# Optimization experiments

Hardware: AMD Instinct MI355X
Metric: run time of the kernel (lower is better)

Reference implementation:

```python
import jax, jax.numpy as jnp
import numpy as np

B, C, N, K, G = 4, 128, 4096, 9, 4


def setup_inputs() -> dict:
    key = jax.random.key(0)
    ks = jax.random.split(key, 4)
    s = 0.05
    return {
        "features": jax.random.normal(ks[0], (B, C, N, 1), jnp.float32),
        # Attn.linear: Conv2d(2C -> C, 1x1)
        "w_lin": jax.random.normal(ks[1], (C, 2 * C), jnp.float32) * s,
        "b_lin": jnp.zeros((C,), jnp.float32),
        # atten_weight_conv: Linear(C -> K*G)
        "w_aw": jax.random.normal(ks[2], (K * G, C), jnp.float32) * s,
        "b_aw": jnp.zeros((K * G,), jnp.float32),
        # GroupNorm(4, C)
        "gn_g": jnp.ones((C,), jnp.float32),
        "gn_b": jnp.zeros((C,), jnp.float32),
        # conv: Conv2d(C -> C, 1x1) + BatchNorm2d(C)
        "conv_w": jax.random.normal(ks[3], (C, C), jnp.float32) * s,
        "conv_b": jnp.zeros((C,), jnp.float32),
        "bn_g": jnp.ones((C,), jnp.float32),
        "bn_b": jnp.zeros((C,), jnp.float32),
    }


def reference(features, w_lin, b_lin, w_aw, b_aw, gn_g, gn_b, conv_w, conv_b, bn_g, bn_b):
    B, C, N, _ = features.shape
    K, G = 9, 4
    Cg = C // G  # 32 channels per group
    EPS = 1e-5

    x = features[..., 0]                       # [B,C,N]
    # ---- KNN graph (negative squared distance, top-k) ----
    xx = jnp.sum(x * x, axis=1)                # [B,N]
    inner = jnp.einsum('bcn,bcm->bnm', x, x)   # [B,N,N]
    pd = 2.0 * inner - xx[:, :, None] - xx[:, None, :]
    idx = jax.lax.top_k(pd, K)[1]              # [B,N,K]

    # ---- edge feature gather: cat(x, x - x_neighbor) ----
    xt = x.transpose(0, 2, 1)                  # [B,N,C]
    b_ix = jnp.arange(B)[:, None, None]
    nbr = xt[b_ix, idx]                        # [B,N,K,C]
    ctr = jnp.broadcast_to(xt[:, :, None, :], (B, N, K, C))
    edge = jnp.concatenate([ctr, ctr - nbr], axis=-1)   # [B,N,K,2C]

    # ---- Attn.linear (1x1 conv == per-position linear) ----
    feat = jnp.einsum('bnke,ce->bnkc', edge, w_lin) + b_lin  # [B,N,K,C]

    # ---- grouped channel attention (4 groups of 32) ----
    fg = feat.reshape(B, N, K, G, Cg)
    scores = jnp.einsum('bnkgc,bnjgc->bngkj', fg, fg) / np.sqrt(32.0)
    s = jax.nn.softmax(scores, axis=-1)        # [B,N,G,K,K]
    attn = jnp.einsum('bngkj,bnjgc->bngkc', s, jax.nn.elu(fg))  # [B,N,G,K,Cg]

    # ---- attention weights over neighbors ----
    aw = jnp.einsum('bnc,dc->bnd', xt, w_aw) + b_aw          # [B,N,K*G]
    aw = jax.nn.softmax(aw.reshape(B, N, G, K), axis=-1)     # [B,N,G,K]

    # ---- weighted neighbor combine ----
    lf = jnp.einsum('bngk,bngkc->bngc', aw, attn)            # [B,N,G,Cg]
    lf = lf.transpose(0, 2, 3, 1).reshape(B, C, N, 1)        # [B,C,N,1]

    # ---- GroupNorm(4, C) over residual ----
    y = lf + features
    yg = y.reshape(B, G, Cg * N)
    mu = yg.mean(-1, keepdims=True)
    var = yg.var(-1, keepdims=True)
    yn = ((yg - mu) / jnp.sqrt(var + EPS)).reshape(B, C, N, 1)
    yn = yn * gn_g[None, :, None, None] + gn_b[None, :, None, None]

    # ---- 1x1 conv + BatchNorm (training-mode batch stats) + ReLU ----
    z = jnp.einsum('oc,bcnk->bonk', conv_w, yn) + conv_b[None, :, None, None]
    m = z.mean(axis=(0, 2, 3), keepdims=True)
    v = z.var(axis=(0, 2, 3), keepdims=True)
    z = (z - m) / jnp.sqrt(v + EPS) * bn_g[None, :, None, None] + bn_b[None, :, None, None]
    return jax.nn.relu(z)
```

## Files before the change

### kernel.cpp

```cpp
#include <hip/hip_runtime.h>
#include <hip/hip_bf16.h>
#include <cstddef>

#define NPTS 4096
#define CCH  128
#define KNN  9
#define GRP  4
#define BB   4
#define OFF_XT    0u
#define OFF_XX    2097152u
#define OFF_XHI   2113536u
#define OFF_IDX   3162112u
#define OFF_O     3309568u
#define OFF_Y     8159232u
#define OFF_GNP   10256384u
#define OFF_GNA   10387456u
#define OFF_GND   10387968u
#define OFF_WP    10388480u
#define OFF_BIASP 10454016u
#define OFF_BNSUM 10454528u
#define OFF_BNSQ  10454656u
#define OFF_BNSC  10454784u
#define OFF_BNSH  10454912u

using bf16x8 = __attribute__((ext_vector_type(8))) short;
using f32x4  = __attribute__((ext_vector_type(4))) float;

#define CE(a, b) { float _h = fmaxf(a, b); b = fminf(a, b); a = _h; }

#define SENT_BITS 0xFF7FF000u

__global__ void k_transpose(const float* __restrict__ x, float* __restrict__ xt,
                            __hip_bfloat16* __restrict__ xhi, float* __restrict__ xx) {
  __shared__ float t[32][33];
  int tx = threadIdx.x, ty = threadIdx.y;
  int n0 = blockIdx.x * 32, c0 = blockIdx.y * 32, b = blockIdx.z;
  float v = x[((size_t)b * CCH + c0 + ty) * NPTS + n0 + tx];
  t[ty][tx] = v;
  __syncthreads();
  float tv = t[tx][ty];
  size_t R = (size_t)b * NPTS + n0 + ty;
  int c = c0 + tx;
  xt[R * CCH + c] = tv;
  int g = c >> 3, w = c & 7;
  int sc = (((g ^ ((n0 + ty) & 15)) << 3) | w);
  xhi[R * CCH + sc] = __float2bfloat16(tv);
  if (ty == 0) {
    float s = 0.f;
    #pragma unroll
    for (int k = 0; k < 32; k++) { float u = t[k][tx]; s += u * u; }
    atomicAdd(&xx[b * NPTS + n0 + tx], s);
  }
}

__device__ __forceinline__ void select_chunk(int c, int wave, int quad,
                                             const f32x4 (&acc)[2][2],
                                             float (&top8)[2][8]) {
  const unsigned cbase = (unsigned)(c * 128 + wave * 32 + quad * 4);
  #pragma unroll
  for (int qt = 0; qt < 2; qt++) {
    float k[8];
    #pragma unroll
    for (int ct = 0; ct < 2; ct++)
      #pragma unroll
      for (int r = 0; r < 4; r++) {
        unsigned u = __float_as_uint(acc[ct][qt][r]);
        k[ct * 4 + r] = __uint_as_float((u & 0xFFFFF000u) |
                                        (cbase + (unsigned)(ct * 16 + r)));
      }
    CE(k[0],k[1]) CE(k[2],k[3]) CE(k[4],k[5]) CE(k[6],k[7])
    CE(k[0],k[2]) CE(k[1],k[3]) CE(k[4],k[6]) CE(k[5],k[7])
    CE(k[1],k[2]) CE(k[5],k[6])
    CE(k[0],k[4]) CE(k[1],k[5]) CE(k[2],k[6]) CE(k[3],k[7])
    CE(k[2],k[4]) CE(k[3],k[5])
    CE(k[1],k[2]) CE(k[3],k[4]) CE(k[5],k[6])
    float t[8];
    #pragma unroll
    for (int i = 0; i < 8; i++) t[i] = fmaxf(top8[qt][i], k[7 - i]);
    CE(t[0],t[4]) CE(t[1],t[5]) CE(t[2],t[6]) CE(t[3],t[7])
    CE(t[0],t[2]) CE(t[1],t[3]) CE(t[4],t[6]) CE(t[5],t[7])
    CE(t[0],t[1]) CE(t[2],t[3]) CE(t[4],t[5]) CE(t[6],t[7])
    #pragma unroll
    for (int i = 0; i < 8; i++) top8[qt][i] = t[i];
  }
}

__device__ __forceinline__ void load_chunk(const short* __restrict__ xb,
                                           const int (&aoff)[2][4], int c,
                                           bf16x8 (&af)[2][4]) {
  const short* cb = xb + c * (128 * CCH);
  #pragma unroll
  for (int ct = 0; ct < 2; ct++)
    #pragma unroll
    for (int ks = 0; ks < 4; ks++)
      af[ct][ks] = *(const bf16x8*)(cb + aoff[ct][ks]);
}

__launch_bounds__(256, 3)
__global__ void k_knn(const short* __restrict__ xhi, const float* __restrict__ xx,
                      float* __restrict__ cand) {
  __shared__ short Qs[32 * 136];
  __shared__ float XXs[1408];
  const int tid = threadIdx.x;
  const int wave = tid >> 6, lane = tid & 63;
  const int quad = lane >> 4, m = lane & 15;
  const int b = blockIdx.y;
  const int q0 = blockIdx.x * 32;
  const int z = blockIdx.z;
  const int ch0 = z * 11;
  const int cnt = (z == 2) ? 10 : 11;
  const short* xb = xhi + (size_t)b * NPTS * CCH;
  const float* xxb = xx + (b << 12);

  {
    int f = tid;
    #pragma unroll
    for (int it = 0; it < 2; it++, f += 256) {
      int row = f >> 4, s = f & 15;
      bf16x8 v = *(const bf16x8*)(xb + (size_t)(q0 + row) * CCH + s * 8);
      int g = s ^ (row & 15);
      *(bf16x8*)&Qs[row * 136 + g * 8] = v;
    }
    const float4* src4 = (const float4*)(xxb + ch0 * 128);
    float4* dst4 = (float4*)XXs;
    int nf4 = cnt * 32;
    for (int i = tid; i < nf4; i += 256) {
      float4 v = src4[i];
      dst4[i] = make_float4(-0.5f * v.x, -0.5f * v.y, -0.5f * v.z, -0.5f * v.w);
    }
  }

  int aoff[2][4];
  #pragma unroll
  for (int ct = 0; ct < 2; ct++)
    #pragma unroll
    for (int ks = 0; ks < 4; ks++)
      aoff[ct][ks] = (wave * 32 + ct * 16 + m) * CCH + (((ks * 4 + quad) ^ m) * 8);

  float top8[2][8];
  #pragma unroll
  for (int qt = 0; qt < 2; qt++)
    #pragma unroll
    for (int p = 0; p < 8; p++) top8[qt][p] = __uint_as_float(SENT_BITS);

  f32x4 acc[2][2];
  bf16x8 bufA[2][4], bufB[2][4];

  unsigned qoff = (unsigned)(m * 272 + quad * 16);
  const unsigned xbase = (unsigned)(wave * 128 + quad * 16);

  load_chunk(xb, aoff, ch0, bufA);
  __syncthreads();

  auto mfma_lds = [&](const bf16x8 (&af)[2][4], int crel) {
    unsigned xo = xbase + (unsigned)crel * 512u;
    f32x4 ci0 = *(const f32x4*)((const char*)XXs + xo);
    f32x4 ci1 = *(const f32x4*)((const char*)XXs + xo + 64);
    acc[0][0] = ci0; acc[0][1] = ci0; acc[1][0] = ci1; acc[1][1] = ci1;
    #pragma unroll
    for (int ks = 0; ks < 4; ks++) {
      bf16x8 qv0 = *(const bf16x8*)((const char*)Qs + qoff + ks * 64);
      bf16x8 qv1 = *(const bf16x8*)((const char*)Qs + qoff + 4352 + ks * 64);
      acc[0][0] = __builtin_amdgcn_mfma_f32_16x16x32_bf16(af[0][ks], qv0, acc[0][0], 0, 0, 0);
      acc[0][1] = __builtin_amdgcn_mfma_f32_16x16x32_bf16(af[0][ks], qv1, acc[0][1], 0, 0, 0);
      acc[1][0] = __builtin_amdgcn_mfma_f32_16x16x32_bf16(af[1][ks], qv0, acc[1][0], 0, 0, 0);
      acc[1][1] = __builtin_amdgcn_mfma_f32_16x16x32_bf16(af[1][ks], qv1, acc[1][1], 0, 0, 0);
    }
  };

  int c = ch0;
  for (; c + 1 < ch0 + cnt; c += 2) {
    load_chunk(xb, aoff, c + 1, bufB);
    if (c > ch0) select_chunk(c - 1, wave, quad, acc, top8);
    asm volatile("" : "+v"(qoff));
    mfma_lds(bufA, c - ch0);
    if (c + 2 < ch0 + cnt) load_chunk(xb, aoff, c + 2, bufA);
    select_chunk(c, wave, quad, acc, top8);
    asm volatile("" : "+v"(qoff));
    mfma_lds(bufB, c + 1 - ch0);
  }
  if (cnt & 1) {
    select_chunk(ch0 + cnt - 2, wave, quad, acc, top8);
    asm volatile("" : "+v"(qoff));
    mfma_lds(bufA, cnt - 1);
  }
  select_chunk(ch0 + cnt - 1, wave, quad, acc, top8);

  int slot = wave * 4 + quad;
  #pragma unroll
  for (int qt = 0; qt < 2; qt++) {
    int q = q0 + qt * 16 + m;
    float* dst = cand + ((size_t)((b << 12) + q) * 48 + z * 16 + slot) * 8;
    #pragma unroll
    for (int p = 0; p < 8; p++) dst[p] = top8[qt][p];
  }
}

__launch_bounds__(256)
__global__ void k_rerank(const float* __restrict__ cand, const float* __restrict__ xt,
                         const float* __restrict__ xx, int* __restrict__ idxOut) {
  __shared__ __align__(16) float arr[4][128];
  __shared__ int selS[4][16];
  __shared__ float keyS[4][16];
  int tid = threadIdx.x, wave = tid >> 6, lane = tid & 63;
  int qg = blockIdx.x * 4 + wave;
  int b = qg >> 12;
  const float* src = cand + (size_t)qg * 384;
  if (lane < 16) {
    const float* pa = src + lane * 8;
    float4 a0 = *(const float4*)pa,         a1 = *(const float4*)(pa + 4);
    float4 b0 = *(const float4*)(pa + 128), b1 = *(const float4*)(pa + 132);
    float4 c0 = *(const float4*)(pa + 256), c1 = *(const float4*)(pa + 260);
    float t[8];
    t[0] = fmaxf(a0.x, b1.w); t[1] = fmaxf(a0.y, b1.z);
    t[2] = fmaxf(a0.z, b1.y); t[3] = fmaxf(a0.w, b1.x);
    t[4] = fmaxf(a1.x, b0.w); t[5] = fmaxf(a1.y, b0.z);
    t[6] = fmaxf(a1.z, b0.y); t[7] = fmaxf(a1.w, b0.x);
    CE(t[0],t[4]) CE(t[1],t[5]) CE(t[2],t[6]) CE(t[3],t[7])
    CE(t[0],t[2]) CE(t[1],t[3]) CE(t[4],t[6]) CE(t[5],t[7])
    CE(t[0],t[1]) CE(t[2],t[3]) CE(t[4],t[5]) CE(t[6],t[7])
    arr[wave][lane * 8 + 0] = fmaxf(t[0], c1.w);
    arr[wave][lane * 8 + 1] = fmaxf(t[1], c1.z);
    arr[wave][lane * 8 + 2] = fmaxf(t[2], c1.y);
    arr[wave][lane * 8 + 3] = fmaxf(t[3], c1.x);
    arr[wave][lane * 8 + 4] = fmaxf(t[4], c0.w);
    arr[wave][lane * 8 + 5] = fmaxf(t[5], c0.z);
    arr[wave][lane * 8 + 6] = fmaxf(t[6], c0.y);
    arr[wave][lane * 8 + 7] = fmaxf(t[7], c0.x);
  }
  __syncthreads();
  float e1 = arr[wave][lane], e2 = arr[wave][lane + 64];
  int r1 = 0, r2 = 0;
  #pragma unroll 8
  for (int f = 0; f < 128; f += 4) {
    float4 fv = *(const float4*)&arr[wave][f];
    r1 += (fv.x > e1) + (fv.y > e1) + (fv.z > e1) + (fv.w > e1);
    r2 += (fv.x > e2) + (fv.y > e2) + (fv.z > e2) + (fv.w > e2);
  }
  if (r1 < 16) selS[wave][r1] = (int)(__float_as_uint(e1) & 0xFFFu);
  if (r2 < 16) selS[wave][r2] = (int)(__float_as_uint(e2) & 0xFFFu);
  __syncthreads();
  int cnum = lane >> 2, part = lane & 3;
  int cidx = selS[wave][cnum];
  const float* rq = xt + (size_t)qg * CCH;
  const float* rc = xt + ((size_t)(b << 12) + cidx) * CCH;
  float dot = 0.f;
  #pragma unroll
  for (int j = 0; j < 8; j++) {
    float4 a4 = *(const float4*)&rq[part * 32 + j * 4];
    float4 c4 = *(const float4*)&rc[part * 32 + j * 4];
    dot += a4.x * c4.x + a4.y * c4.y + a4.z * c4.z + a4.w * c4.w;
  }
  dot += __shfl_xor(dot, 1);
  dot += __shfl_xor(dot, 2);
  if (part == 0)
    keyS[wave][cnum] = fmaf(2.f, dot, -xx[(b << 12) + cidx]);
  __syncthreads();
  if (lane < 16) {
    float k = keyS[wave][lane]; int i = selS[wave][lane];
    int r = 0;
    #pragma unroll
    for (int f = 0; f < 16; f++) {
      float fk = keyS[wave][f]; int fi = selS[wave][f];
      r += (fk > k) || (fk == k && fi < i);
    }
    if (r < 9) idxOut[(size_t)qg * 9 + r] = i;
  }
}

__launch_bounds__(256)
__global__ void k_linear(const float* __restrict__ xt, const float* __restrict__ w_lin,
                         const float* __restrict__ b_lin, const float* __restrict__ w_aw,
                         const float* __restrict__ b_aw, float* __restrict__ O) {
  __shared__ __align__(16) float Xs[64 * 132];
  __shared__ __align__(16) float Ws[64 * 132];
  int tid = threadIdx.x;
  int tx = tid & 15, ty = tid >> 4;
  int p0 = blockIdx.x * 64, o0 = blockIdx.y * 64;
  #pragma unroll
  for (int i = 0; i < 8; i++) {
    int flat = tid + i * 256; int r = flat >> 5, c4 = flat & 31;
    *(float4*)&Xs[r * 132 + c4 * 4] = *(const float4*)&xt[(size_t)(p0 + r) * CCH + c4 * 4];
  }
  #pragma unroll
  for (int i = 0; i < 8; i++) {
    int flat = tid + i * 256; int r = flat >> 5, c4 = flat & 31;
    int o = o0 + r; float4 v;
    if (o < 128) {
      float4 a = *(const float4*)&w_lin[(size_t)o * 256 + c4 * 4];
      float4 c = *(const float4*)&w_lin[(size_t)o * 256 + 128 + c4 * 4];
      v = make_float4(a.x + c.x, a.y + c.y, a.z + c.z, a.w + c.w);
    } else if (o < 256) {
      v = *(const float4*)&w_lin[(size_t)(o - 128) * 256 + 128 + c4 * 4];
    } else if (o < 292) {
      v = *(const float4*)&w_aw[(size_t)(o - 256) * 128 + c4 * 4];
    } else v = make_float4(0.f, 0.f, 0.f, 0.f);
    *(float4*)&Ws[r * 132 + c4 * 4] = v;
  }
  __syncthreads();
  float acc[4][4] = {};
  #pragma unroll 2
  for (int kq = 0; kq < 32; kq++) {
    float4 xa[4], wb[4];
    #pragma unroll
    for (int i = 0; i < 4; i++) xa[i] = *(const float4*)&Xs[(ty * 4 + i) * 132 + kq * 4];
    #pragma unroll
    for (int j = 0; j < 4; j++) wb[j] = *(const float4*)&Ws[(tx + 16 * j) * 132 + kq * 4];
    #pragma unroll
    for (int i = 0; i < 4; i++)
      #pragma unroll
      for (int j = 0; j < 4; j++)
        acc[i][j] += xa[i].x * wb[j].x + xa[i].y * wb[j].y + xa[i].z * wb[j].z + xa[i].w * wb[j].w;
  }
  #pragma unroll
  for (int j = 0; j < 4; j++) {
    int o = o0 + tx + 16 * j;
    if (o < 292) {
      float bias = (o < 128) ? b_lin[o] : ((o < 256) ? 0.f : b_aw[o - 256]);
      #pragma unroll
      for (int i = 0; i < 4; i++)
        O[(size_t)(p0 + ty * 4 + i) * 296 + o] = acc[i][j] + bias;
    }
  }
}

__launch_bounds__(256)
__global__ void k_attn(const float* __restrict__ O, const int* __restrict__ idxArr,
                       const float* __restrict__ xt, float* __restrict__ Y,
                       float* __restrict__ gnPart) {
  __shared__ __align__(16) float fF[4][1188];
  __shared__ __align__(16) float scS[4][432];
  __shared__ float awS[4][48];
  __shared__ float w9S[4][48];
  __shared__ int tI[45], tJ[45];
  int tid = threadIdx.x;
  int wave = tid >> 6, l = tid & 63;
  int pos = blockIdx.x * 4 + wave;
  int b = pos >> 12;
  if (tid == 0) {
    int p = 0;
    for (int i = 0; i < 9; i++) for (int j = i; j < 9; j++) { tI[p] = i; tJ[p] = j; p++; }
  }
  int nbr[9];
  const float* Op = O + (size_t)pos * 296;
  #pragma unroll
  for (int k = 0; k < 9; k++) nbr[k] = idxArr[(size_t)pos * 9 + k];
  float2 u = *(const float2*)(Op + 2 * l);
  float* fFw = fF[wave];
  #pragma unroll
  for (int k = 0; k < 9; k++) {
    const float* vp = O + (size_t)((b << 12) + nbr[k]) * 296 + 128;
    float2 vv = *(const float2*)(vp + 2 * l);
    *(float2*)&fFw[k * 132 + 2 * l] = make_float2(u.x - vv.x, u.y - vv.y);
  }
  __syncthreads();
  #pragma unroll
  for (int r = 0; r < 3; r++) {
    int p = r * 64 + l;
    if (p < 180) {
      int g = p / 45, q = p - g * 45;
      int i = tI[q], j = tJ[q];
      const float* fi = fFw + i * 132 + g * 32;
      const float* fj = fFw + j * 132 + g * 32;
      float s = 0.f;
      #pragma unroll
      for (int t8 = 0; t8 < 8; t8++) {
        float4 a4 = *(const float4*)(fi + 4 * t8);
        float4 b4 = *(const float4*)(fj + 4 * t8);
        s += a4.x * b4.x + a4.y * b4.y + a4.z * b4.z + a4.w * b4.w;
      }
      s *= 0.17677669529663687f;
      scS[wave][(g * 9 + i) * 12 + j] = s;
      scS[wave][(g * 9 + j) * 12 + i] = s;
    }
  }
  __syncthreads();
  if (l < 36) {
    int g = l / 9, i = l - g * 9;
    float* rp = &scS[wave][(g * 9 + i) * 12];
    float mx = rp[0];
    #pragma unroll
    for (int j = 1; j < 9; j++) mx = fmaxf(mx, rp[j]);
    float e[9]; float sm = 0.f;
    #pragma unroll
    for (int j = 0; j < 9; j++) { e[j] = __expf(rp[j] - mx); sm += e[j]; }
    float inv = 1.f / sm;
    #pragma unroll
    for (int j = 0; j < 9; j++) rp[j] = e[j] * inv;
  } else if (l < 40) {
    int g = l - 36;
    float a[9]; float mx = -3.4e38f;
    #pragma unroll
    for (int k = 0; k < 9; k++) { a[k] = Op[256 + g * 9 + k]; mx = fmaxf(mx, a[k]); }
    float sm = 0.f;
    #pragma unroll
    for (int k = 0; k < 9; k++) { a[k] = __expf(a[k] - mx); sm += a[k]; }
    float inv = 1.f / sm;
    #pragma unroll
    for (int k = 0; k < 9; k++) awS[wave][g * 12 + k] = a[k] * inv;
  }
  __syncthreads();
  if (l < 36) {
    int g = l / 9, j = l - g * 9;
    float s = 0.f;
    #pragma unroll
    for (int i = 0; i < 9; i++) s += awS[wave][g * 12 + i] * scS[wave][(g * 9 + i) * 12 + j];
    w9S[wave][g * 12 + j] = s;
  }
  __syncthreads();
  int g = l >> 4;
  float w9r[9];
  #pragma unroll
  for (int j = 0; j < 9; j++) w9r[j] = w9S[wave][g * 12 + j];
  int c0 = 2 * l;
  float lf0 = 0.f, lf1 = 0.f;
  #pragma unroll
  for (int j = 0; j < 9; j++) {
    float2 f2 = *(const float2*)&fFw[j * 132 + c0];
    float e0 = f2.x > 0.f ? f2.x : __expf(f2.x) - 1.f;
    float e1 = f2.y > 0.f ? f2.y : __expf(f2.y) - 1.f;
    lf0 += w9r[j] * e0;
    lf1 += w9r[j] * e1;
  }
  float2 xv = *(const float2*)(xt + (size_t)pos * CCH + c0);
  float y0 = lf0 + xv.x, y1 = lf1 + xv.y;
  *(float2*)(Y + (size_t)pos * CCH + c0) = make_float2(y0, y1);
  float s1 = y0 + y1, s2 = y0 * y0 + y1 * y1;
  #pragma unroll
  for (int mm = 1; mm <= 8; mm <<= 1) { s1 += __shfl_xor(s1, mm); s2 += __shfl_xor(s2, mm); }
  if ((l & 15) == 0) {
    gnPart[(size_t)pos * 8 + g * 2]     = s1;
    gnPart[(size_t)pos * 8 + g * 2 + 1] = s2;
  }
}

__global__ void k_gnstats(const float* __restrict__ gnPart,
                          const float* __restrict__ gn_g, const float* __restrict__ gn_b,
                          float* __restrict__ gnA, float* __restrict__ gnD) {
  int bg = blockIdx.x; int b = bg >> 2, g = bg & 3;
  int tid = threadIdx.x;
  float s1 = 0.f, s2 = 0.f;
  for (int r = tid; r < NPTS; r += 256) {
    const float* p = gnPart + (size_t)(b * NPTS + r) * 8 + g * 2;
    s1 += p[0]; s2 += p[1];
  }
  __shared__ float r1[256], r2[256];
  r1[tid] = s1; r2[tid] = s2;
  __syncthreads();
  for (int off = 128; off > 0; off >>= 1) {
    if (tid < off) { r1[tid] += r1[tid + off]; r2[tid] += r2[tid + off]; }
    __syncthreads();
  }
  __shared__ float muS, rsS;
  if (tid == 0) {
    float mu = r1[0] * (1.f / 131072.f);
    float var = r2[0] * (1.f / 131072.f) - mu * mu;
    muS = mu; rsS = 1.f / sqrtf(var + 1e-5f);
  }
  __syncthreads();
  if (tid < 32) {
    int c = g * 32 + tid;
    float a = rsS * gn_g[c];
    gnA[b * 128 + c] = a;
    gnD[b * 128 + c] = gn_b[c] - muS * a;
  }
}

__global__ void k_fold(const float* __restrict__ conv_w, const float* __restrict__ conv_b,
                       const float* __restrict__ gnA, const float* __restrict__ gnD,
                       float* __restrict__ Wp, float* __restrict__ biasp) {
  int b = blockIdx.x; int tid = threadIdx.x;
  __shared__ float dS[128], aS[128];
  if (tid < 128) { dS[tid] = gnD[b * 128 + tid]; aS[tid] = gnA[b * 128 + tid]; }
  __syncthreads();
  for (int f = tid; f < 16384; f += 256)
    Wp[(size_t)b * 16384 + f] = conv_w[f] * aS[f & 127];
  if (tid < 128) {
    float s = conv_b[tid];
    for (int c = 0; c < 128; c++) s += conv_w[tid * 128 + c] * dS[c];
    biasp[b * 128 + tid] = s;
  }
}

__launch_bounds__(256)
__global__ void k_conv(const float* __restrict__ Y, const float* __restrict__ Wp,
                       const float* __restrict__ biasp, float* __restrict__ zpre,
                       float* __restrict__ bnSum, float* __restrict__ bnSq) {
  __shared__ __align__(16) float Ys[64 * 132];
  __shared__ __align__(16) float Ws[64 * 132];
  int tid = threadIdx.x;
  int tx = tid & 15, ty = tid >> 4;
  int n0 = blockIdx.x * 64, o0 = blockIdx.y * 64, b = blockIdx.z;
  #pragma unroll
  for (int i = 0; i < 8; i++) {
    int flat = tid + i * 256; int r = flat >> 5, c4 = flat & 31;
    *(float4*)&Ys[r * 132 + c4 * 4] = *(const float4*)&Y[(size_t)((b << 12) + n0 + r) * CCH + c4 * 4];
    *(float4*)&Ws[r * 132 + c4 * 4] = *(const float4*)&Wp[(size_t)b * 16384 + (size_t)(o0 + r) * 128 + c4 * 4];
  }
  __syncthreads();
  float acc[4][4] = {};
  #pragma unroll 2
  for (int kq = 0; kq < 32; kq++) {
    float4 wa[4], yb[4];
    #pragma unroll
    for (int i = 0; i < 4; i++) wa[i] = *(const float4*)&Ws[(ty * 4 + i) * 132 + kq * 4];
    #pragma unroll
    for (int j = 0; j < 4; j++) yb[j] = *(const float4*)&Ys[(tx + 16 * j) * 132 + kq * 4];
    #pragma unroll
    for (int i = 0; i < 4; i++)
      #pragma unroll
      for (int j = 0; j < 4; j++)
        acc[i][j] += wa[i].x * yb[j].x + wa[i].y * yb[j].y + wa[i].z * yb[j].z + wa[i].w * yb[j].w;
  }
  #pragma unroll
  for (int i = 0; i < 4; i++) {
    int o = o0 + ty * 4 + i;
    float bias = biasp[b * 128 + o];
    float p1 = 0.f, p2 = 0.f;
    #pragma unroll
    for (int j = 0; j < 4; j++) {
      float z = acc[i][j] + bias;
      zpre[(((size_t)((b << 7) + o)) << 12) + n0 + tx + 16 * j] = z;
      p1 += z; p2 += z * z;
    }
    #pragma unroll
    for (int mm = 1; mm <= 8; mm <<= 1) { p1 += __shfl_xor(p1, mm); p2 += __shfl_xor(p2, mm); }
    if (tx == 0) { atomicAdd(&bnSum[o], p1); atomicAdd(&bnSq[o], p2); }
  }
}

__global__ void k_bnfin(const float* __restrict__ bnSum, const float* __restrict__ bnSq,
                        const float* __restrict__ bn_g, const float* __restrict__ bn_b,
                        float* __restrict__ bnScale, float* __restrict__ bnShift) {
  int o = threadIdx.x;
  float m = bnSum[o] * (1.f / 16384.f);
  float v = bnSq[o] * (1.f / 16384.f) - m * m;
  float sc = bn_g[o] / sqrtf(v + 1e-5f);
  bnScale[o] = sc;
  bnShift[o] = bn_b[o] - m * sc;
}

__global__ void k_final(const float* __restrict__ zpre, const float* __restrict__ bnScale,
                        const float* __restrict__ bnShift, float* __restrict__ out) {
  int i4 = blockIdx.x * 256 + threadIdx.x;
  int e = i4 * 4;
  int o = (e >> 12) & 127;
  float4 z = *(const float4*)&zpre[e];
  float sc = bnScale[o], sh = bnShift[o];
  float4 r;
  r.x = fmaxf(fmaf(z.x, sc, sh), 0.f);
  r.y = fmaxf(fmaf(z.y, sc, sh), 0.f);
  r.z = fmaxf(fmaf(z.z, sc, sh), 0.f);
  r.w = fmaxf(fmaf(z.w, sc, sh), 0.f);
  *(float4*)&out[e] = r;
}

extern "C" void kernel_launch(void* const* d_in, const int* in_sizes, int n_in,
                              void* d_out, int out_size, void* d_ws, size_t ws_size,
                              hipStream_t stream) {
  const float* features = (const float*)d_in[0];
  const float* w_lin  = (const float*)d_in[1];
  const float* b_lin  = (const float*)d_in[2];
  const float* w_aw   = (const float*)d_in[3];
  const float* b_aw   = (const float*)d_in[4];
  const float* gn_g   = (const float*)d_in[5];
  const float* gn_b   = (const float*)d_in[6];
  const float* conv_w = (const float*)d_in[7];
  const float* conv_b = (const float*)d_in[8];
  const float* bn_g   = (const float*)d_in[9];
  const float* bn_b   = (const float*)d_in[10];

  float* ws    = (float*)d_ws;
  float* xt    = ws + OFF_XT;
  float* xxp   = ws + OFF_XX;
  __hip_bfloat16* xhip = (__hip_bfloat16*)(ws + OFF_XHI);
  int*   idxp  = (int*)(ws + OFF_IDX);
  float* Op    = ws + OFF_O;
  float* candp = ws + OFF_O;
  float* Yp    = ws + OFF_Y;
  float* gnp   = ws + OFF_GNP;
  float* gnA   = ws + OFF_GNA;
  float* gnD   = ws + OFF_GND;
  float* Wp    = ws + OFF_WP;
  float* biasp = ws + OFF_BIASP;
  float* bnSum = ws + OFF_BNSUM;
  float* bnSq  = ws + OFF_BNSQ;
  float* bnSc  = ws + OFF_BNSC;
  float* bnSh  = ws + OFF_BNSH;
  float* zpre  = xt;

  hipMemsetAsync(xxp, 0, NPTS * BB * sizeof(float), stream);
  hipMemsetAsync(bnSum, 0, 256 * sizeof(float), stream);

  k_transpose<<<dim3(128, 4, 4), dim3(32, 32), 0, stream>>>(features, xt, xhip, xxp);
  k_knn<<<dim3(128, 4, 3), 256, 0, stream>>>((const short*)xhip, xxp, candp);
  k_rerank<<<4096, 256, 0, stream>>>(candp, xt, xxp, idxp);
  k_linear<<<dim3(256, 5), 256, 0, stream>>>(xt, w_lin, b_lin, w_aw, b_aw, Op);
  k_attn<<<4096, 256, 0, stream>>>(Op, idxp, xt, Yp, gnp);
  k_gnstats<<<16, 256, 0, stream>>>(gnp, gn_g, gn_b, gnA, gnD);
  k_fold<<<4, 256, 0, stream>>>(conv_w, conv_b, gnA, gnD, Wp, biasp);
  k_conv<<<dim3(64, 2, 4), 256, 0, stream>>>(Yp, Wp, biasp, zpre, bnSum, bnSq);
  k_bnfin<<<1, 128, 0, stream>>>(bnSum, bnSq, bn_g, bn_b, bnSc, bnSh);
  k_final<<<2048, 256, 0, stream>>>(zpre, bnSc, bnSh, (float*)d_out);
}
```

Measured before the change: 271.3 us.

## Merge per-quad top-8 candidates in-register before writing, shrink rerank candidate list

```diff
diff --git a/kernel.cpp b/kernel.cpp
--- a/kernel.cpp
+++ b/kernel.cpp
@@ -28,6 +28,16 @@
 
 #define CE(a, b) { float _h = fmaxf(a, b); b = fminf(a, b); a = _h; }
 
+#define BMERGE16(s) \
+  CE(s[0],s[8])  CE(s[1],s[9])  CE(s[2],s[10]) CE(s[3],s[11]) \
+  CE(s[4],s[12]) CE(s[5],s[13]) CE(s[6],s[14]) CE(s[7],s[15]) \
+  CE(s[0],s[4])  CE(s[1],s[5])  CE(s[2],s[6])  CE(s[3],s[7])  \
+  CE(s[8],s[12]) CE(s[9],s[13]) CE(s[10],s[14]) CE(s[11],s[15]) \
+  CE(s[0],s[2])  CE(s[1],s[3])  CE(s[4],s[6])  CE(s[5],s[7])  \
+  CE(s[8],s[10]) CE(s[9],s[11]) CE(s[12],s[14]) CE(s[13],s[15]) \
+  CE(s[0],s[1])  CE(s[2],s[3])  CE(s[4],s[5])  CE(s[6],s[7])  \
+  CE(s[8],s[9])  CE(s[10],s[11]) CE(s[12],s[13]) CE(s[14],s[15])
+
 #define SENT_BITS 0xFF7FF000u
 
 __global__ void k_transpose(const float* __restrict__ x, float* __restrict__ xt,
@@ -186,59 +196,55 @@
   }
   select_chunk(ch0 + cnt - 1, wave, quad, acc, top8);
 
-  int slot = wave * 4 + quad;
   #pragma unroll
   for (int qt = 0; qt < 2; qt++) {
-    int q = q0 + qt * 16 + m;
-    float* dst = cand + ((size_t)((b << 12) + q) * 48 + z * 16 + slot) * 8;
-    #pragma unroll
-    for (int p = 0; p < 8; p++) dst[p] = top8[qt][p];
+    float s[16];
+    #pragma unroll
+    for (int i = 0; i < 8; i++) {
+      s[i] = top8[qt][i];
+      s[15 - i] = __shfl_xor(top8[qt][i], 16);
+    }
+    BMERGE16(s)
+    float t[16];
+    #pragma unroll
+    for (int i = 0; i < 16; i++) t[i] = fmaxf(s[i], __shfl_xor(s[15 - i], 32));
+    BMERGE16(t)
+    if (quad == 0) {
+      int q = q0 + qt * 16 + m;
+      float* dst = cand + ((size_t)((b << 12) + q) * 192 + (size_t)(z * 4 + wave) * 16);
+      *(float4*)&dst[0]  = make_float4(t[0],  t[1],  t[2],  t[3]);
+      *(float4*)&dst[4]  = make_float4(t[4],  t[5],  t[6],  t[7]);
+      *(float4*)&dst[8]  = make_float4(t[8],  t[9],  t[10], t[11]);
+      *(float4*)&dst[12] = make_float4(t[12], t[13], t[14], t[15]);
+    }
   }
 }
 
 __launch_bounds__(256)
 __global__ void k_rerank(const float* __restrict__ cand, const float* __restrict__ xt,
                          const float* __restrict__ xx, int* __restrict__ idxOut) {
-  __shared__ __align__(16) float arr[4][128];
+  __shared__ __align__(16) float runS[4][192];
   __shared__ int selS[4][16];
   __shared__ float keyS[4][16];
   int tid = threadIdx.x, wave = tid >> 6, lane = tid & 63;
   int qg = blockIdx.x * 4 + wave;
   int b = qg >> 12;
-  const float* src = cand + (size_t)qg * 384;
+  const float* src = cand + (size_t)qg * 192;
+  if (lane < 48) *(float4*)&runS[wave][lane * 4] = *(const float4*)&src[lane * 4];
+  __syncthreads();
   if (lane < 16) {
-    const float* pa = src + lane * 8;
-    float4 a0 = *(const float4*)pa,         a1 = *(const float4*)(pa + 4);
-    float4 b0 = *(const float4*)(pa + 128), b1 = *(const float4*)(pa + 132);
-    float4 c0 = *(const float4*)(pa + 256), c1 = *(const float4*)(pa + 260);
-    float t[8];
-    t[0] = fmaxf(a0.x, b1.w); t[1] = fmaxf(a0.y, b1.z);
-    t[2] = fmaxf(a0.z, b1.y); t[3] = fmaxf(a0.w, b1.x);
-    t[4] = fmaxf(a1.x, b0.w); t[5] = fmaxf(a1.y, b0.z);
-    t[6] = fmaxf(a1.z, b0.y); t[7] = fmaxf(a1.w, b0.x);
-    CE(t[0],t[4]) CE(t[1],t[5]) CE(t[2],t[6]) CE(t[3],t[7])
-    CE(t[0],t[2]) CE(t[1],t[3]) CE(t[4],t[6]) CE(t[5],t[7])
-    CE(t[0],t[1]) CE(t[2],t[3]) CE(t[4],t[5]) CE(t[6],t[7])
-    arr[wave][lane * 8 + 0] = fmaxf(t[0], c1.w);
-    arr[wave][lane * 8 + 1] = fmaxf(t[1], c1.z);
-    arr[wave][lane * 8 + 2] = fmaxf(t[2], c1.y);
-    arr[wave][lane * 8 + 3] = fmaxf(t[3], c1.x);
-    arr[wave][lane * 8 + 4] = fmaxf(t[4], c0.w);
-    arr[wave][lane * 8 + 5] = fmaxf(t[5], c0.z);
-    arr[wave][lane * 8 + 6] = fmaxf(t[6], c0.y);
-    arr[wave][lane * 8 + 7] = fmaxf(t[7], c0.x);
-  }
-  __syncthreads();
-  float e1 = arr[wave][lane], e2 = arr[wave][lane + 64];
-  int r1 = 0, r2 = 0;
-  #pragma unroll 8
-  for (int f = 0; f < 128; f += 4) {
-    float4 fv = *(const float4*)&arr[wave][f];
-    r1 += (fv.x > e1) + (fv.y > e1) + (fv.z > e1) + (fv.w > e1);
-    r2 += (fv.x > e2) + (fv.y > e2) + (fv.z > e2) + (fv.w > e2);
-  }
-  if (r1 < 16) selS[wave][r1] = (int)(__float_as_uint(e1) & 0xFFFu);
-  if (r2 < 16) selS[wave][r2] = (int)(__float_as_uint(e2) & 0xFFFu);
+    float t = runS[wave][lane];
+    #pragma unroll
+    for (int r = 1; r < 12; r++) {
+      t = fmaxf(t, runS[wave][r * 16 + (15 - lane)]);
+      #pragma unroll
+      for (int d = 8; d >= 1; d >>= 1) {
+        float o = __shfl_xor(t, d);
+        t = (lane & d) ? fminf(t, o) : fmaxf(t, o);
+      }
+    }
+    selS[wave][lane] = (int)(__float_as_uint(t) & 0xFFFu);
+  }
   __syncthreads();
   int cnum = lane >> 2, part = lane & 3;
   int cidx = selS[wave][cnum];
```

After: 273.8 us. About the same (+0.9%).
